# Performance work log

Hardware: AMD Instinct MI355X
Metric: run time of the kernel (lower is better)

Reference implementation:

```python
import jax, jax.numpy as jnp
import numpy as np

WINDOW_SIZE = 11
SIGMA = 1.5
CHANNEL = 3
L = 2.0
C1 = (0.01 * L) ** 2
C2 = (0.03 * L) ** 2
WEIGHTS = jnp.asarray([0.0448, 0.2856, 0.3001, 0.2363, 0.1333], dtype=jnp.float32)


def _create_window(window_size=WINDOW_SIZE, channel=CHANNEL):
    x = jnp.arange(window_size, dtype=jnp.float32)
    g = jnp.exp(-((x - window_size // 2) ** 2) / (2.0 * SIGMA ** 2))
    g = g / g.sum()
    w2d = jnp.outer(g, g)  # (ws, ws)
    # depthwise kernel, OIHW with I=1, O=channel
    return jnp.broadcast_to(w2d[None, None], (channel, 1, window_size, window_size))


def _depthwise_conv(x, w):
    # x: (B,C,H,W), w: (C,1,kh,kw), groups=C, VALID padding
    return jax.lax.conv_general_dilated(
        x, w, window_strides=(1, 1), padding='VALID',
        feature_group_count=x.shape[1],
        dimension_numbers=('NCHW', 'OIHW', 'NCHW'))


def _ssim_level(img1, img2, window):
    mu1 = _depthwise_conv(img1, window)
    mu2 = _depthwise_conv(img2, window)
    mu1_sq = mu1 * mu1
    mu2_sq = mu2 * mu2
    mu1_mu2 = mu1 * mu2
    sigma1_sq = _depthwise_conv(img1 * img1, window) - mu1_sq
    sigma2_sq = _depthwise_conv(img2 * img2, window) - mu2_sq
    sigma12 = _depthwise_conv(img1 * img2, window) - mu1_mu2
    v1 = 2.0 * sigma12 + C2
    v2 = sigma1_sq + sigma2_sq + C2
    cs = jnp.mean(v1 / v2)
    ssim_map = (2.0 * mu1_mu2 + C1) * v1 / ((mu1_sq + mu2_sq + C1) * v2)
    return jnp.mean(ssim_map), cs


def _avg_pool2(x):
    b, c, h, w = x.shape
    return x.reshape(b, c, h // 2, 2, w // 2, 2).mean(axis=(3, 5))


def _msssim(img1, img2):
    window = _create_window()
    mssim, mcs = [], []
    for _ in range(WEIGHTS.shape[0]):
        sim, cs = _ssim_level(img1, img2, window)
        mssim.append(sim)
        mcs.append(cs)
        img1 = _avg_pool2(img1)
        img2 = _avg_pool2(img2)
    mssim = jnp.stack(mssim)
    mcs = jnp.stack(mcs)
    # normalize=True
    mssim = (mssim + 1.0) / 2.0
    mcs = (mcs + 1.0) / 2.0
    pow1 = mcs ** WEIGHTS
    pow2 = mssim ** WEIGHTS
    # faithful to source: prod over broadcast of pow1[:-1] * pow2[-1]
    return jnp.prod(pow1[:-1] * pow2[-1])


def setup_inputs() -> dict:
    key = jax.random.key(0)
    k1, k2 = jax.random.split(key)
    shape = (16, 3, 512, 512)
    output = jax.random.uniform(k1, shape, dtype=jnp.float32)
    gt = jax.random.uniform(k2, shape, dtype=jnp.float32)
    return {"output": output, "gt": gt}


def reference(output, gt):
    return 1.0 - _msssim(output, gt)
```

## Files before the change

### kernel.cpp

```cpp
#include <hip/hip_runtime.h>
#include <math.h>

typedef float vf2 __attribute__((ext_vector_type(2)));

__device__ __forceinline__ vf2 pk_fma(vf2 a, vf2 b, vf2 c) {
    vf2 d;
    asm("v_pk_fma_f32 %0, %1, %2, %3" : "=v"(d) : "v"(a), "v"(b), "v"(c));
    return d;
}
__device__ __forceinline__ vf2 pk_mul(vf2 a, vf2 b) {
    vf2 d;
    asm("v_pk_mul_f32 %0, %1, %2" : "=v"(d) : "v"(a), "v"(b));
    return d;
}
__device__ __forceinline__ vf2 pk_fma_blo(vf2 w, vf2 b, vf2 c) {
    vf2 d;
    asm("v_pk_fma_f32 %0, %1, %2, %3 op_sel_hi:[0,1,1]"
        : "=v"(d) : "v"(w), "v"(b), "v"(c));
    return d;
}
__device__ __forceinline__ vf2 pk_fma_bhi(vf2 w, vf2 b, vf2 c) {
    vf2 d;
    asm("v_pk_fma_f32 %0, %1, %2, %3 op_sel:[1,0,0] op_sel_hi:[1,1,1]"
        : "=v"(d) : "v"(w), "v"(b), "v"(c));
    return d;
}

#define L0_H 512
#define L0_HOUT 502
#define L0_HP 256
#define L0_SEG 64
#define L0_NCHUNK 7
#define ROWW 536
#define NQ 134
#define CARRY_BASE (11 * ROWW)
#define STREAM_WORDS (CARRY_BASE + 2 * ROWW)

__global__ __launch_bounds__(256)
void msssim_stream_l0(const float* __restrict__ img1,
                      const float* __restrict__ img2,
                      double* __restrict__ sums,
                      float* __restrict__ poolP, float* __restrict__ poolQ)
{
    __shared__ __align__(16) float buf[STREAM_WORDS];
    __shared__ float wred[4][2];

    const float gs[11] = {0.00102838f, 0.00759875f, 0.03600077f, 0.10936070f,
                          0.21300554f, 0.26601173f, 0.21300554f, 0.10936070f,
                          0.03600077f, 0.00759875f, 0.00102838f};

    const int tid = threadIdx.x;
    const int c0 = blockIdx.x * 256;
    const int oy0 = blockIdx.y * L0_SEG;
    const long long plane = (long long)blockIdx.z * L0_H * L0_H;
    const long long pplane = (long long)blockIdx.z * L0_HP * L0_HP;
    const bool colok = (c0 + tid) < L0_HOUT;

    const int par = tid & 1;
    vf2 wp[6];
    #pragma unroll
    for (int jq = 0; jq < 6; ++jq) {
        const int i0 = 2 * jq, i1 = 2 * jq + 1;
        const float we0 = (i0 < 11) ? gs[i0] : 0.f;
        const float wo0 = (i0 >= 1) ? gs[i0 - 1] : 0.f;
        const float we1 = (i1 < 11) ? gs[i1] : 0.f;
        const float wo1 = (i1 >= 1) ? gs[i1 - 1] : 0.f;
        wp[jq].x = par ? wo0 : we0;
        wp[jq].y = par ? wo1 : we1;
    }
    vf2 wgv[6];
    #pragma unroll
    for (int k = 0; k < 6; ++k) { wgv[k].x = gs[k]; wgv[k].y = gs[k]; }

    int rowS[6], colS[6], ldsoff[6], rHS[6];
    #pragma unroll
    for (int t = 0; t < 6; ++t) {
        const int s = tid + 256 * t;
        if (s < 11 * NQ) {
            const int r = s / NQ, q = s - NQ * r;
            rowS[t] = r;
            colS[t] = c0 + 2 * q;
            ldsoff[t] = r * ROWW + q * 4;
            rHS[t] = r * L0_H;
        } else { rowS[t] = -1; colS[t] = 0; ldsoff[t] = 0; rHS[t] = 0; }
    }

    float4 pf[6];
    auto prefetch = [&](int ybase) {
        const int yH = ybase * L0_H;
        #pragma unroll
        for (int t = 0; t < 6; ++t) {
            float2 a = make_float2(0.f, 0.f), b = make_float2(0.f, 0.f);
            if (rowS[t] >= 0) {
                const int y = ybase + rowS[t];
                if (y < L0_H && colS[t] < L0_H) {
                    const long long idx = plane + yH + rHS[t] + colS[t];
                    a = *(const float2*)(img1 + idx);
                    b = *(const float2*)(img2 + idx);
                }
            }
            pf[t] = make_float4(a.x + b.x, a.x - b.x, a.y + b.y, a.y - b.y);
        }
    };
    auto stage_write = [&]() {
        #pragma unroll
        for (int t = 0; t < 6; ++t)
            if (rowS[t] >= 0) *(float4*)&buf[ldsoff[t]] = pf[t];
    };

    prefetch(oy0);
    stage_write();
    __syncthreads();

    vf2 pd_pq[11], pd_sq[11];
    #pragma unroll
    for (int s = 0; s < 11; ++s) { pd_pq[s] = (vf2){0.f, 0.f}; pd_sq[s] = (vf2){0.f, 0.f}; }

    const int qb4 = (tid >> 1) * 4;
    const float C1 = 4.0e-4f, C2 = 3.6e-3f;
    float ssim_acc = 0.f, cs_acc = 0.f;

    for (int c = 0; c < L0_NCHUNK; ++c) {
        const int cs = oy0 + 11 * c;
        const bool more = (c + 1 < L0_NCHUNK);

        if (more) prefetch(cs + 11);

        if (tid < 128) {
            const int px = (c0 >> 1) + tid;
            const int t4 = tid * 4;
            for (int jp = (cs & 1); jp + 1 <= 10; jp += 2) {
                const int py = (cs + jp) >> 1;
                if (py < L0_HP) {
                    const float4 v0 = *(const float4*)&buf[jp * ROWW + t4];
                    const float4 v1 = *(const float4*)&buf[(jp + 1) * ROWW + t4];
                    poolP[pplane + py * L0_HP + px] = 0.25f * (v0.x + v0.z + v1.x + v1.z);
                    poolQ[pplane + py * L0_HP + px] = 0.25f * (v0.y + v0.w + v1.y + v1.w);
                }
            }
            if (c > 0 && (cs & 1)) {
                const int py = (cs - 1) >> 1;
                if (py < L0_HP) {
                    const float4 v0 = *(const float4*)&buf[CARRY_BASE + ((c - 1) & 1) * ROWW + t4];
                    const float4 v1 = *(const float4*)&buf[t4];
                    poolP[pplane + py * L0_HP + px] = 0.25f * (v0.x + v0.z + v1.x + v1.z);
                    poolQ[pplane + py * L0_HP + px] = 0.25f * (v0.y + v0.w + v1.y + v1.w);
                }
            }
        }
        if (((cs & 1) == 0) && more && tid < NQ) {
            *(float4*)&buf[CARRY_BASE + (c & 1) * ROWW + tid * 4] =
                *(const float4*)&buf[10 * ROWW + tid * 4];
        }

        #pragma unroll
        for (int j = 0; j < 11; ++j) {
            pd_pq[j] = (vf2){0.f, 0.f};
            pd_sq[j] = (vf2){0.f, 0.f};

            float4 q[6];
            const int rw = j * ROWW + qb4;
            #pragma unroll
            for (int u = 0; u < 6; ++u) q[u] = *(const float4*)&buf[rw + 4 * u];

            vf2 hpq = {0.f, 0.f}, hsq = {0.f, 0.f};
            #pragma unroll
            for (int u = 0; u < 6; ++u) {
                const vf2 elo = {q[u].x, q[u].y};
                const vf2 ehi = {q[u].z, q[u].w};
                const vf2 slo = pk_mul(elo, elo);
                const vf2 shi = pk_mul(ehi, ehi);
                hpq = pk_fma_blo(wp[u], elo, hpq);
                hpq = pk_fma_bhi(wp[u], ehi, hpq);
                hsq = pk_fma_blo(wp[u], slo, hsq);
                hsq = pk_fma_bhi(wp[u], shi, hsq);
            }
            #pragma unroll
            for (int k = 0; k < 11; ++k) {
                const int s = (j - k + 11) % 11;
                const int m = (k <= 5) ? k : 10 - k;
                pd_pq[s] = pk_fma(wgv[m], hpq, pd_pq[s]);
                pd_sq[s] = pk_fma(wgv[m], hsq, pd_sq[s]);
            }
            const int yrel = 11 * c + j;
            if (yrel >= 10) {
                const int s = (j + 1) % 11;
                const int orow = yrel - 10;
                if (orow < L0_SEG && (oy0 + orow) < L0_HOUT && colok) {
                    const vf2 musq = pk_mul(pd_pq[s], pd_pq[s]);
                    const float sP = pd_sq[s].x - musq.x;
                    const float sQ = pd_sq[s].y - musq.y;
                    const float v1 = 0.5f * (sP - sQ) + C2;
                    const float v2 = 0.5f * (sP + sQ) + C2;
                    const float num1 = 0.5f * (musq.x - musq.y) + C1;
                    const float den1 = 0.5f * (musq.x + musq.y) + C1;
                    cs_acc += v1 * __builtin_amdgcn_rcpf(v2);
                    ssim_acc += num1 * v1 * __builtin_amdgcn_rcpf(den1 * v2);
                }
            }
        }

        __syncthreads();
        if (more) stage_write();
        __syncthreads();
    }

    #pragma unroll
    for (int off = 32; off > 0; off >>= 1) {
        ssim_acc += __shfl_down(ssim_acc, off);
        cs_acc   += __shfl_down(cs_acc, off);
    }
    const int wave = tid >> 6;
    if ((tid & 63) == 0) { wred[wave][0] = ssim_acc; wred[wave][1] = cs_acc; }
    __syncthreads();
    if (tid == 0) {
        atomicAdd(&sums[0], (double)(wred[0][0] + wred[1][0] + wred[2][0] + wred[3][0]));
        atomicAdd(&sums[5], (double)(wred[0][1] + wred[1][1] + wred[2][1] + wred[3][1]));
    }
}

#define TILE 32
#define IN_DIM 42
#define SCP 21
#define HALO 10
#define STAGE_WORDS (IN_DIM * SCP * 4)
#define SH 340
#define HB STAGE_WORDS
#define SMEM_WORDS (HB + 16 * SH)

__global__ __launch_bounds__(256)
void msssim_level_kernel(const float* __restrict__ src1,
                         const float* __restrict__ src2,
                         int H, int level, int tiles_per_seg, int pq_input,
                         double* __restrict__ sums,
                         float* __restrict__ pool1, float* __restrict__ pool2)
{
    __shared__ __align__(16) float smem[SMEM_WORDS];
    __shared__ float wred[4][2];

    const float g[11] = {0.00102838f, 0.00759875f, 0.03600077f, 0.10936070f,
                         0.21300554f, 0.26601173f, 0.21300554f, 0.10936070f,
                         0.03600077f, 0.00759875f, 0.00102838f};
    vf2 wg[11];
    #pragma unroll
    for (int k = 0; k < 11; ++k) { wg[k].x = g[k]; wg[k].y = g[k]; }

    const int tid = threadIdx.x;
    const int Hout = H - HALO;
    const int ntiles = (Hout + TILE - 1) / TILE;
    const int tstart = blockIdx.y * tiles_per_seg;
    const int tend = min(ntiles, tstart + tiles_per_seg);
    const int ox0 = blockIdx.x * TILE;
    const int Hp = H >> 1;
    const long long base = (long long)blockIdx.z * H * H;

    int rHS[4], rS[4], xS[4];
    #pragma unroll
    for (int t4 = 0; t4 < 4; ++t4) {
        const int s = tid + 256 * t4;
        if (s < IN_DIM * SCP) {
            const int r = s / SCP, cp = s - r * SCP;
            rS[t4] = r; rHS[t4] = r * H; xS[t4] = ox0 + 2 * cp;
        } else { rS[t4] = -1; rHS[t4] = 0; xS[t4] = 0; }
    }

    auto load_slot = [&](int t4, int ybase) -> float4 {
        float2 a = make_float2(0.f, 0.f), b = make_float2(0.f, 0.f);
        if (rS[t4] >= 0) {
            const int y = ybase + rS[t4], x = xS[t4];
            if (y < H && x < H) {
                const long long idx = base + (long long)ybase * H + rHS[t4] + x;
                a = *(const float2*)(src1 + idx);
                b = *(const float2*)(src2 + idx);
            }
        }
        if (pq_input) return make_float4(a.x, b.x, a.y, b.y);
        return make_float4(a.x + b.x, a.x - b.x, a.y + b.y, a.y - b.y);
    };

    float4 pref[4];
    {
        #pragma unroll
        for (int t4 = 0; t4 < 4; ++t4) pref[t4] = load_slot(t4, tstart * TILE);
        #pragma unroll
        for (int t4 = 0; t4 < 4; ++t4)
            if (rS[t4] >= 0) *(float4*)&smem[(tid + 256 * t4) * 4] = pref[t4];
    }
    __syncthreads();

    float ssim_acc = 0.f, cs_acc = 0.f;

    for (int tt = tstart; tt < tend; ++tt) {
        const int ty0 = tt * TILE;
        const bool more = (tt + 1 < tend);

        if (more) {
            #pragma unroll
            for (int t4 = 0; t4 < 4; ++t4) pref[t4] = load_slot(t4, ty0 + TILE);
        }

        if (pool1 != nullptr) {
            const int pr = tid >> 4, pc = tid & 15;
            const int py = (ty0 >> 1) + pr, px = (ox0 >> 1) + pc;
            if (py < Hp && px < Hp) {
                const float4 v0 = *(const float4*)&smem[(2 * pr * SCP + pc) * 4];
                const float4 v1 = *(const float4*)&smem[((2 * pr + 1) * SCP + pc) * 4];
                const long long ob = (long long)blockIdx.z * Hp * Hp + (long long)py * Hp + px;
                pool1[ob] = 0.25f * (v0.x + v0.z + v1.x + v1.z);
                pool2[ob] = 0.25f * (v0.y + v0.w + v1.y + v1.w);
            }
        }

        float4 hA[3], hBv[3];
        #pragma unroll
        for (int t = 0; t < 3; ++t) {
            const int p = tid + 256 * t;
            if (p < IN_DIM * 16) {
                const int r = p >> 4, m = p & 15;
                vf2 Apq = {0.f, 0.f}, Asq = {0.f, 0.f};
                vf2 Bpq = {0.f, 0.f}, Bsq = {0.f, 0.f};
                #pragma unroll
                for (int jj = 0; jj < 6; ++jj) {
                    const float4 v = *(const float4*)&smem[(r * SCP + m + jj) * 4];
                    const vf2 lo = {v.x, v.y};
                    const vf2 hi = {v.z, v.w};
                    const vf2 losq = pk_mul(lo, lo);
                    const vf2 hisq = pk_mul(hi, hi);
                    Apq = pk_fma(wg[2 * jj], lo, Apq);
                    Asq = pk_fma(wg[2 * jj], losq, Asq);
                    if (jj >= 1) {
                        Bpq = pk_fma(wg[2 * jj - 1], lo, Bpq);
                        Bsq = pk_fma(wg[2 * jj - 1], losq, Bsq);
                    }
                    if (jj <= 4) {
                        Apq = pk_fma(wg[2 * jj + 1], hi, Apq);
                        Asq = pk_fma(wg[2 * jj + 1], hisq, Asq);
                    }
                    Bpq = pk_fma(wg[2 * jj], hi, Bpq);
                    Bsq = pk_fma(wg[2 * jj], hisq, Bsq);
                }
                hA[t]  = make_float4(Apq.x, Apq.y, Asq.x, Asq.y);
                hBv[t] = make_float4(Bpq.x, Bpq.y, Bsq.x, Bsq.y);
            }
        }
        __syncthreads();

        #pragma unroll
        for (int t = 0; t < 3; ++t) {
            const int p = tid + 256 * t;
            if (p < IN_DIM * 16) {
                const int r = p >> 4, m = p & 15;
                const int hb = HB + m * SH + r * 8;
                *(float4*)&smem[hb]     = hA[t];
                *(float4*)&smem[hb + 4] = hBv[t];
            }
        }
        if (more) {
            #pragma unroll
            for (int t4 = 0; t4 < 4; ++t4)
                if (rS[t4] >= 0) *(float4*)&smem[(tid + 256 * t4) * 4] = pref[t4];
        }
        __syncthreads();

        const int tx = tid & 31, rg = tid >> 5;
        const int r0 = rg * 4;
        const int m = tx >> 1, par = tx & 1;
        const int hb = HB + m * SH + par * 4;

        vf2 accPQ[4], accSQ[4];
        #pragma unroll
        for (int o = 0; o < 4; ++o) {
            accPQ[o] = (vf2){0.f, 0.f};
            accSQ[o] = (vf2){0.f, 0.f};
        }
        #pragma unroll
        for (int i = 0; i < 14; ++i) {
            const float4 h4 = *(const float4*)&smem[hb + (r0 + i) * 8];
            const vf2 ppq = {h4.x, h4.y};
            const vf2 psq = {h4.z, h4.w};
            #pragma unroll
            for (int o = 0; o < 4; ++o) {
                const int k = i - o;
                if (k >= 0 && k <= 10) {
                    accPQ[o] = pk_fma(wg[k], ppq, accPQ[o]);
                    accSQ[o] = pk_fma(wg[k], psq, accSQ[o]);
                }
            }
        }

        const float C1 = 4.0e-4f;
        const float C2 = 3.6e-3f;
        const int ox = ox0 + tx;
        #pragma unroll
        for (int o = 0; o < 4; ++o) {
            const int oy = ty0 + r0 + o;
            if (oy < Hout && ox < Hout) {
                const vf2 musq = pk_mul(accPQ[o], accPQ[o]);
                const float sP = accSQ[o].x - musq.x;
                const float sQ = accSQ[o].y - musq.y;
                const float v1 = 0.5f * (sP - sQ) + C2;
                const float v2 = 0.5f * (sP + sQ) + C2;
                const float num1 = 0.5f * (musq.x - musq.y) + C1;
                const float den1 = 0.5f * (musq.x + musq.y) + C1;
                cs_acc += v1 * __builtin_amdgcn_rcpf(v2);
                ssim_acc += num1 * v1 * __builtin_amdgcn_rcpf(den1 * v2);
            }
        }
    }

    #pragma unroll
    for (int off = 32; off > 0; off >>= 1) {
        ssim_acc += __shfl_down(ssim_acc, off);
        cs_acc   += __shfl_down(cs_acc, off);
    }
    const int wave = tid >> 6;
    if ((tid & 63) == 0) { wred[wave][0] = ssim_acc; wred[wave][1] = cs_acc; }
    __syncthreads();
    if (tid == 0) {
        const float s = wred[0][0] + wred[1][0] + wred[2][0] + wred[3][0];
        const float c = wred[0][1] + wred[1][1] + wred[2][1] + wred[3][1];
        atomicAdd(&sums[level],     (double)s);
        atomicAdd(&sums[5 + level], (double)c);
    }
}

__global__ void msssim_final_kernel(const double* __restrict__ sums,
                                    float* __restrict__ out)
{
    if (threadIdx.x == 0 && blockIdx.x == 0) {
        const double W[5] = {0.0448, 0.2856, 0.3001, 0.2363, 0.1333};
        const int Houts[5] = {502, 246, 118, 54, 22};
        double mssim[5], mcs[5];
        for (int l = 0; l < 5; ++l) {
            const double cnt = 48.0 * (double)Houts[l] * (double)Houts[l];
            mssim[l] = (sums[l]     / cnt + 1.0) * 0.5;
            mcs[l]   = (sums[5 + l] / cnt + 1.0) * 0.5;
        }
        const double p2 = pow(mssim[4], W[4]);
        double prod = 1.0;
        for (int l = 0; l < 4; ++l) prod *= pow(mcs[l], W[l]) * p2;
        out[0] = (float)(1.0 - prod);
    }
}

extern "C" void kernel_launch(void* const* d_in, const int* in_sizes, int n_in,
                              void* d_out, int out_size, void* d_ws, size_t ws_size,
                              hipStream_t stream)
{
    const float* img1 = (const float*)d_in[0];
    const float* img2 = (const float*)d_in[1];
    float* out = (float*)d_out;
    (void)in_sizes; (void)n_in; (void)out_size; (void)ws_size;

    char* ws = (char*)d_ws;
    double* sums = (double*)ws;
    float* X1 = (float*)(ws + 256);
    float* X2 = X1 + 3145728;
    float* Y1 = X2 + 3145728;
    float* Y2 = Y1 + 786432;

    hipMemsetAsync(sums, 0, 10 * sizeof(double), stream);

    hipLaunchKernelGGL(msssim_stream_l0, dim3(2, 8, 48), dim3(256), 0, stream,
                       img1, img2, sums, X1, X2);

    auto launch_level = [&](const float* a, const float* b, int H, int level,
                            int segs, float* pa, float* pb) {
        const int Hout = H - HALO;
        const int strips = (Hout + TILE - 1) / TILE;
        const int ntiles = (Hout + TILE - 1) / TILE;
        const int tps = (ntiles + segs - 1) / segs;
        dim3 grid(strips, segs, 48);
        hipLaunchKernelGGL(msssim_level_kernel, grid, dim3(256), 0, stream,
                           a, b, H, level, tps, 1, sums, pa, pb);
    };

    launch_level(X1, X2, 256, 1, 2, Y1, Y2);
    launch_level(Y1, Y2, 128, 2, 4, X1, X2);
    launch_level(X1, X2, 64, 3, 2, Y1, Y2);
    launch_level(Y1, Y2, 32, 4, 1, nullptr, nullptr);

    hipLaunchKernelGGL(msssim_final_kernel, dim3(1), dim3(64), 0, stream, sums, out);
}
```

Before: 142.7 us.

## Precompute pyramid in one cascade kernel and run all SSIM levels in one launch

Replaces the chain of per-level launches with two kernels. The first computes every pooled pyramid level from the inputs in one pass, using shared memory for the intermediate levels. The second is a single launch whose blocks are split across all five SSIM levels, with level 1 pooling directly from the full-resolution inputs. This removes serial launch dependencies and the small, low-occupancy launches for the coarse levels. In exchange the inputs are read again by the cascade kernel and by level 1, and the grid mixes blocks with very different amounts of work.

Measured after the change: 129.8 us. -9.1%, faster.

```diff
diff --git a/kernel.cpp b/kernel.cpp
--- a/kernel.cpp
+++ b/kernel.cpp
@@ -28,168 +28,381 @@
 
 #define L0_H 512
 #define L0_HOUT 502
-#define L0_HP 256
 #define L0_SEG 64
 #define L0_NCHUNK 7
 #define ROWW 536
 #define NQ 134
-#define CARRY_BASE (11 * ROWW)
-#define STREAM_WORDS (CARRY_BASE + 2 * ROWW)
+#define L0_BUF (11 * ROWW)
+
+#define TILE 32
+#define IN_DIM 42
+#define SCP 21
+#define HALO 10
+#define LV_STAGE (IN_DIM * SCP * 4)
+#define SH 340
+#define HB LV_STAGE
+#define MEGA_WORDS (HB + 16 * SH)
 
 __global__ __launch_bounds__(256)
-void msssim_stream_l0(const float* __restrict__ img1,
-                      const float* __restrict__ img2,
-                      double* __restrict__ sums,
-                      float* __restrict__ poolP, float* __restrict__ poolQ)
+void msssim_cascade(const float* __restrict__ img1, const float* __restrict__ img2,
+                    float* __restrict__ Y1, float* __restrict__ Y2,
+                    float* __restrict__ Z1, float* __restrict__ Z2,
+                    float* __restrict__ W1, float* __restrict__ W2)
 {
-    __shared__ __align__(16) float buf[STREAM_WORDS];
+    __shared__ float xs[16 * 256 * 2];
+    __shared__ float ysh[8 * 128 * 2];
+    __shared__ float zsh[4 * 64 * 2];
+    const int tid = threadIdx.x;
+    const int reg = blockIdx.x & 15, plane = blockIdx.x >> 4;
+    const long long obase = (long long)plane * 262144;
+
+    for (int i = tid; i < 16 * 256; i += 256) {
+        const int r = i >> 8, c = i & 255;
+        const long long o = obase + (long long)(2 * (16 * reg + r)) * 512 + 2 * c;
+        const float2 a0 = *(const float2*)&img1[o];
+        const float2 a1 = *(const float2*)&img1[o + 512];
+        const float2 b0 = *(const float2*)&img2[o];
+        const float2 b1 = *(const float2*)&img2[o + 512];
+        xs[2 * i]     = 0.25f * ((a0.x + b0.x) + (a0.y + b0.y) + (a1.x + b1.x) + (a1.y + b1.y));
+        xs[2 * i + 1] = 0.25f * ((a0.x - b0.x) + (a0.y - b0.y) + (a1.x - b1.x) + (a1.y - b1.y));
+    }
+    __syncthreads();
+    for (int i = tid; i < 8 * 128; i += 256) {
+        const int r = i >> 7, c = i & 127;
+        const int i00 = ((2 * r) * 256 + 2 * c) * 2;
+        const float yP = 0.25f * (xs[i00] + xs[i00 + 2] + xs[i00 + 512] + xs[i00 + 514]);
+        const float yQ = 0.25f * (xs[i00 + 1] + xs[i00 + 3] + xs[i00 + 513] + xs[i00 + 515]);
+        ysh[2 * i] = yP; ysh[2 * i + 1] = yQ;
+        const long long yo = (long long)plane * 16384 + (long long)(8 * reg + r) * 128 + c;
+        Y1[yo] = yP; Y2[yo] = yQ;
+    }
+    __syncthreads();
+    for (int i = tid; i < 4 * 64; i += 256) {
+        const int r = i >> 6, c = i & 63;
+        const int i00 = ((2 * r) * 128 + 2 * c) * 2;
+        const float zP = 0.25f * (ysh[i00] + ysh[i00 + 2] + ysh[i00 + 256] + ysh[i00 + 258]);
+        const float zQ = 0.25f * (ysh[i00 + 1] + ysh[i00 + 3] + ysh[i00 + 257] + ysh[i00 + 259]);
+        zsh[2 * i] = zP; zsh[2 * i + 1] = zQ;
+        const long long zo = (long long)plane * 4096 + (long long)(4 * reg + r) * 64 + c;
+        Z1[zo] = zP; Z2[zo] = zQ;
+    }
+    __syncthreads();
+    for (int i = tid; i < 2 * 32; i += 256) {
+        const int r = i >> 5, c = i & 31;
+        const int i00 = ((2 * r) * 64 + 2 * c) * 2;
+        const long long wo = (long long)plane * 1024 + (long long)(2 * reg + r) * 32 + c;
+        W1[wo] = 0.25f * (zsh[i00] + zsh[i00 + 2] + zsh[i00 + 128] + zsh[i00 + 130]);
+        W2[wo] = 0.25f * (zsh[i00 + 1] + zsh[i00 + 3] + zsh[i00 + 129] + zsh[i00 + 131]);
+    }
+}
+
+__global__ __launch_bounds__(256)
+void msssim_mega(const float* __restrict__ img1, const float* __restrict__ img2,
+                 const float* __restrict__ Y1, const float* __restrict__ Y2,
+                 const float* __restrict__ Z1, const float* __restrict__ Z2,
+                 const float* __restrict__ W1, const float* __restrict__ W2,
+                 double* __restrict__ sums)
+{
+    __shared__ __align__(16) float smem[MEGA_WORDS];
     __shared__ float wred[4][2];
 
     const float gs[11] = {0.00102838f, 0.00759875f, 0.03600077f, 0.10936070f,
                           0.21300554f, 0.26601173f, 0.21300554f, 0.10936070f,
                           0.03600077f, 0.00759875f, 0.00102838f};
-
     const int tid = threadIdx.x;
-    const int c0 = blockIdx.x * 256;
-    const int oy0 = blockIdx.y * L0_SEG;
-    const long long plane = (long long)blockIdx.z * L0_H * L0_H;
-    const long long pplane = (long long)blockIdx.z * L0_HP * L0_HP;
-    const bool colok = (c0 + tid) < L0_HOUT;
-
-    const int par = tid & 1;
-    vf2 wp[6];
-    #pragma unroll
-    for (int jq = 0; jq < 6; ++jq) {
-        const int i0 = 2 * jq, i1 = 2 * jq + 1;
-        const float we0 = (i0 < 11) ? gs[i0] : 0.f;
-        const float wo0 = (i0 >= 1) ? gs[i0 - 1] : 0.f;
-        const float we1 = (i1 < 11) ? gs[i1] : 0.f;
-        const float wo1 = (i1 >= 1) ? gs[i1 - 1] : 0.f;
-        wp[jq].x = par ? wo0 : we0;
-        wp[jq].y = par ? wo1 : we1;
-    }
-    vf2 wgv[6];
-    #pragma unroll
-    for (int k = 0; k < 6; ++k) { wgv[k].x = gs[k]; wgv[k].y = gs[k]; }
-
-    int rowS[6], colS[6], ldsoff[6], rHS[6];
-    #pragma unroll
-    for (int t = 0; t < 6; ++t) {
-        const int s = tid + 256 * t;
-        if (s < 11 * NQ) {
-            const int r = s / NQ, q = s - NQ * r;
-            rowS[t] = r;
-            colS[t] = c0 + 2 * q;
-            ldsoff[t] = r * ROWW + q * 4;
-            rHS[t] = r * L0_H;
-        } else { rowS[t] = -1; colS[t] = 0; ldsoff[t] = 0; rHS[t] = 0; }
-    }
-
-    float4 pf[6];
-    auto prefetch = [&](int ybase) {
-        const int yH = ybase * L0_H;
-        #pragma unroll
-        for (int t = 0; t < 6; ++t) {
-            float2 a = make_float2(0.f, 0.f), b = make_float2(0.f, 0.f);
-            if (rowS[t] >= 0) {
-                const int y = ybase + rowS[t];
-                if (y < L0_H && colS[t] < L0_H) {
-                    const long long idx = plane + yH + rHS[t] + colS[t];
-                    a = *(const float2*)(img1 + idx);
-                    b = *(const float2*)(img2 + idx);
-                }
-            }
-            pf[t] = make_float4(a.x + b.x, a.x - b.x, a.y + b.y, a.y - b.y);
-        }
-    };
-    auto stage_write = [&]() {
-        #pragma unroll
-        for (int t = 0; t < 6; ++t)
-            if (rowS[t] >= 0) *(float4*)&buf[ldsoff[t]] = pf[t];
-    };
-
-    prefetch(oy0);
-    stage_write();
-    __syncthreads();
-
-    vf2 pd_pq[11], pd_sq[11];
-    #pragma unroll
-    for (int s = 0; s < 11; ++s) { pd_pq[s] = (vf2){0.f, 0.f}; pd_sq[s] = (vf2){0.f, 0.f}; }
-
-    const int qb4 = (tid >> 1) * 4;
+    const int bid = blockIdx.x;
     const float C1 = 4.0e-4f, C2 = 3.6e-3f;
     float ssim_acc = 0.f, cs_acc = 0.f;
-
-    for (int c = 0; c < L0_NCHUNK; ++c) {
-        const int cs = oy0 + 11 * c;
-        const bool more = (c + 1 < L0_NCHUNK);
-
-        if (more) prefetch(cs + 11);
-
-        if (tid < 128) {
-            const int px = (c0 >> 1) + tid;
-            const int t4 = tid * 4;
-            for (int jp = (cs & 1); jp + 1 <= 10; jp += 2) {
-                const int py = (cs + jp) >> 1;
-                if (py < L0_HP) {
-                    const float4 v0 = *(const float4*)&buf[jp * ROWW + t4];
-                    const float4 v1 = *(const float4*)&buf[(jp + 1) * ROWW + t4];
-                    poolP[pplane + py * L0_HP + px] = 0.25f * (v0.x + v0.z + v1.x + v1.z);
-                    poolQ[pplane + py * L0_HP + px] = 0.25f * (v0.y + v0.w + v1.y + v1.w);
-                }
-            }
-            if (c > 0 && (cs & 1)) {
-                const int py = (cs - 1) >> 1;
-                if (py < L0_HP) {
-                    const float4 v0 = *(const float4*)&buf[CARRY_BASE + ((c - 1) & 1) * ROWW + t4];
-                    const float4 v1 = *(const float4*)&buf[t4];
-                    poolP[pplane + py * L0_HP + px] = 0.25f * (v0.x + v0.z + v1.x + v1.z);
-                    poolQ[pplane + py * L0_HP + px] = 0.25f * (v0.y + v0.w + v1.y + v1.w);
-                }
-            }
-        }
-        if (((cs & 1) == 0) && more && tid < NQ) {
-            *(float4*)&buf[CARRY_BASE + (c & 1) * ROWW + tid * 4] =
-                *(const float4*)&buf[10 * ROWW + tid * 4];
-        }
-
-        #pragma unroll
-        for (int j = 0; j < 11; ++j) {
-            pd_pq[j] = (vf2){0.f, 0.f};
-            pd_sq[j] = (vf2){0.f, 0.f};
-
-            float4 q[6];
-            const int rw = j * ROWW + qb4;
-            #pragma unroll
-            for (int u = 0; u < 6; ++u) q[u] = *(const float4*)&buf[rw + 4 * u];
-
-            vf2 hpq = {0.f, 0.f}, hsq = {0.f, 0.f};
-            #pragma unroll
-            for (int u = 0; u < 6; ++u) {
-                const vf2 elo = {q[u].x, q[u].y};
-                const vf2 ehi = {q[u].z, q[u].w};
-                const vf2 slo = pk_mul(elo, elo);
-                const vf2 shi = pk_mul(ehi, ehi);
-                hpq = pk_fma_blo(wp[u], elo, hpq);
-                hpq = pk_fma_bhi(wp[u], ehi, hpq);
-                hsq = pk_fma_blo(wp[u], slo, hsq);
-                hsq = pk_fma_bhi(wp[u], shi, hsq);
-            }
-            #pragma unroll
-            for (int k = 0; k < 11; ++k) {
-                const int s = (j - k + 11) % 11;
-                const int m = (k <= 5) ? k : 10 - k;
-                pd_pq[s] = pk_fma(wgv[m], hpq, pd_pq[s]);
-                pd_sq[s] = pk_fma(wgv[m], hsq, pd_sq[s]);
-            }
-            const int yrel = 11 * c + j;
-            if (yrel >= 10) {
-                const int s = (j + 1) % 11;
-                const int orow = yrel - 10;
-                if (orow < L0_SEG && (oy0 + orow) < L0_HOUT && colok) {
-                    const vf2 musq = pk_mul(pd_pq[s], pd_pq[s]);
-                    const float sP = pd_sq[s].x - musq.x;
-                    const float sQ = pd_sq[s].y - musq.y;
+    int level;
+
+    if (bid < 768) {
+        level = 0;
+        const int c0 = (bid & 1) * 256;
+        const int oy0 = ((bid >> 1) & 7) * L0_SEG;
+        const long long plane = (long long)(bid >> 4) * 262144;
+        const bool colok = (c0 + tid) < L0_HOUT;
+
+        const int par = tid & 1;
+        vf2 wp[6];
+        #pragma unroll
+        for (int jq = 0; jq < 6; ++jq) {
+            const int i0 = 2 * jq, i1 = 2 * jq + 1;
+            const float we0 = (i0 < 11) ? gs[i0] : 0.f;
+            const float wo0 = (i0 >= 1) ? gs[i0 - 1] : 0.f;
+            const float we1 = (i1 < 11) ? gs[i1] : 0.f;
+            const float wo1 = (i1 >= 1) ? gs[i1 - 1] : 0.f;
+            wp[jq].x = par ? wo0 : we0;
+            wp[jq].y = par ? wo1 : we1;
+        }
+        vf2 wgv[6];
+        #pragma unroll
+        for (int k = 0; k < 6; ++k) { wgv[k].x = gs[k]; wgv[k].y = gs[k]; }
+
+        int rowS[6], colS[6], ldsoff[6], rHS[6];
+        #pragma unroll
+        for (int t = 0; t < 6; ++t) {
+            const int s = tid + 256 * t;
+            if (s < 11 * NQ) {
+                const int r = s / NQ, q = s - NQ * r;
+                rowS[t] = r; colS[t] = c0 + 2 * q;
+                ldsoff[t] = r * ROWW + q * 4; rHS[t] = r * L0_H;
+            } else { rowS[t] = -1; colS[t] = 0; ldsoff[t] = 0; rHS[t] = 0; }
+        }
+
+        float4 pf[6];
+        auto prefetch = [&](int ybase) {
+            const int yH = ybase * L0_H;
+            #pragma unroll
+            for (int t = 0; t < 6; ++t) {
+                float2 a = make_float2(0.f, 0.f), b = make_float2(0.f, 0.f);
+                if (rowS[t] >= 0) {
+                    const int y = ybase + rowS[t];
+                    if (y < L0_H && colS[t] < L0_H) {
+                        const long long idx = plane + yH + rHS[t] + colS[t];
+                        a = *(const float2*)(img1 + idx);
+                        b = *(const float2*)(img2 + idx);
+                    }
+                }
+                pf[t] = make_float4(a.x + b.x, a.x - b.x, a.y + b.y, a.y - b.y);
+            }
+        };
+        auto stage_write = [&]() {
+            #pragma unroll
+            for (int t = 0; t < 6; ++t)
+                if (rowS[t] >= 0) *(float4*)&smem[ldsoff[t]] = pf[t];
+        };
+
+        prefetch(oy0);
+        stage_write();
+        __syncthreads();
+
+        vf2 pd_pq[11], pd_sq[11];
+        #pragma unroll
+        for (int s = 0; s < 11; ++s) { pd_pq[s] = (vf2){0.f, 0.f}; pd_sq[s] = (vf2){0.f, 0.f}; }
+
+        const int qb4 = (tid >> 1) * 4;
+
+        for (int c = 0; c < L0_NCHUNK; ++c) {
+            const bool more = (c + 1 < L0_NCHUNK);
+            if (more) prefetch(oy0 + 11 * (c + 1));
+
+            #pragma unroll
+            for (int j = 0; j < 11; ++j) {
+                pd_pq[j] = (vf2){0.f, 0.f};
+                pd_sq[j] = (vf2){0.f, 0.f};
+
+                float4 q[6];
+                const int rw = j * ROWW + qb4;
+                #pragma unroll
+                for (int u = 0; u < 6; ++u) q[u] = *(const float4*)&smem[rw + 4 * u];
+
+                vf2 hpq = {0.f, 0.f}, hsq = {0.f, 0.f};
+                #pragma unroll
+                for (int u = 0; u < 6; ++u) {
+                    const vf2 elo = {q[u].x, q[u].y};
+                    const vf2 ehi = {q[u].z, q[u].w};
+                    const vf2 slo = pk_mul(elo, elo);
+                    const vf2 shi = pk_mul(ehi, ehi);
+                    hpq = pk_fma_blo(wp[u], elo, hpq);
+                    hpq = pk_fma_bhi(wp[u], ehi, hpq);
+                    hsq = pk_fma_blo(wp[u], slo, hsq);
+                    hsq = pk_fma_bhi(wp[u], shi, hsq);
+                }
+                #pragma unroll
+                for (int k = 0; k < 11; ++k) {
+                    const int s = (j - k + 11) % 11;
+                    const int m = (k <= 5) ? k : 10 - k;
+                    pd_pq[s] = pk_fma(wgv[m], hpq, pd_pq[s]);
+                    pd_sq[s] = pk_fma(wgv[m], hsq, pd_sq[s]);
+                }
+                const int yrel = 11 * c + j;
+                if (yrel >= 10) {
+                    const int s = (j + 1) % 11;
+                    const int orow = yrel - 10;
+                    if (orow < L0_SEG && (oy0 + orow) < L0_HOUT && colok) {
+                        const vf2 musq = pk_mul(pd_pq[s], pd_pq[s]);
+                        const float sP = pd_sq[s].x - musq.x;
+                        const float sQ = pd_sq[s].y - musq.y;
+                        const float v1 = 0.5f * (sP - sQ) + C2;
+                        const float v2 = 0.5f * (sP + sQ) + C2;
+                        const float num1 = 0.5f * (musq.x - musq.y) + C1;
+                        const float den1 = 0.5f * (musq.x + musq.y) + C1;
+                        cs_acc += v1 * __builtin_amdgcn_rcpf(v2);
+                        ssim_acc += num1 * v1 * __builtin_amdgcn_rcpf(den1 * v2);
+                    }
+                }
+            }
+
+            __syncthreads();
+            if (more) stage_write();
+            __syncthreads();
+        }
+    } else {
+        const int id = bid - 768;
+        const float *src1 = nullptr, *src2 = nullptr;
+        int H, strip, seg, plane, tps;
+        if (id < 768) {
+            level = 1; H = 256; tps = 4;
+            plane = id >> 4; const int t = id & 15; strip = t & 7; seg = t >> 3;
+        } else if (id < 1536) {
+            level = 2; H = 128; tps = 1; src1 = Y1; src2 = Y2;
+            const int r = id - 768; plane = r >> 4; const int t = r & 15; strip = t & 3; seg = t >> 2;
+        } else if (id < 1728) {
+            level = 3; H = 64; tps = 1; src1 = Z1; src2 = Z2;
+            const int r = id - 1536; plane = r >> 2; const int t = r & 3; strip = t & 1; seg = t >> 1;
+        } else {
+            level = 4; H = 32; tps = 1; src1 = W1; src2 = W2;
+            plane = id - 1728; strip = 0; seg = 0;
+        }
+
+        vf2 wg[11];
+        #pragma unroll
+        for (int k = 0; k < 11; ++k) { wg[k].x = gs[k]; wg[k].y = gs[k]; }
+
+        const int Hout = H - HALO;
+        const int ntiles = (Hout + TILE - 1) / TILE;
+        const int tstart = seg * tps;
+        const int tend = min(ntiles, tstart + tps);
+        const int ox0 = strip * TILE;
+        const long long base = (long long)plane * H * H;
+        const long long obase = (long long)plane * 262144;
+
+        int rHS[4], rS[4], xS[4];
+        #pragma unroll
+        for (int t4 = 0; t4 < 4; ++t4) {
+            const int s = tid + 256 * t4;
+            if (s < IN_DIM * SCP) {
+                const int r = s / SCP, cp = s - r * SCP;
+                rS[t4] = r; rHS[t4] = r * H; xS[t4] = ox0 + 2 * cp;
+            } else { rS[t4] = -1; rHS[t4] = 0; xS[t4] = 0; }
+        }
+
+        auto load_slot = [&](int t4, int ybase) -> float4 {
+            if (rS[t4] < 0) return make_float4(0.f, 0.f, 0.f, 0.f);
+            const int y = ybase + rS[t4], x = xS[t4];
+            if (y >= H || x >= H) return make_float4(0.f, 0.f, 0.f, 0.f);
+            if (level == 1) {
+                const long long o = obase + (long long)(2 * y) * 512 + 2 * x;
+                const float4 A0 = *(const float4*)(img1 + o);
+                const float4 A1 = *(const float4*)(img1 + o + 512);
+                const float4 B0 = *(const float4*)(img2 + o);
+                const float4 B1 = *(const float4*)(img2 + o + 512);
+                const float P0 = 0.25f * ((A0.x + B0.x) + (A0.y + B0.y) + (A1.x + B1.x) + (A1.y + B1.y));
+                const float Q0 = 0.25f * ((A0.x - B0.x) + (A0.y - B0.y) + (A1.x - B1.x) + (A1.y - B1.y));
+                const float P1 = 0.25f * ((A0.z + B0.z) + (A0.w + B0.w) + (A1.z + B1.z) + (A1.w + B1.w));
+                const float Q1 = 0.25f * ((A0.z - B0.z) + (A0.w - B0.w) + (A1.z - B1.z) + (A1.w - B1.w));
+                return make_float4(P0, Q0, P1, Q1);
+            }
+            const long long idx = base + (long long)ybase * H + rHS[t4] + x;
+            const float2 a = *(const float2*)(src1 + idx);
+            const float2 b = *(const float2*)(src2 + idx);
+            return make_float4(a.x, b.x, a.y, b.y);
+        };
+
+        float4 pref[4];
+        {
+            #pragma unroll
+            for (int t4 = 0; t4 < 4; ++t4) pref[t4] = load_slot(t4, tstart * TILE);
+            #pragma unroll
+            for (int t4 = 0; t4 < 4; ++t4)
+                if (rS[t4] >= 0) *(float4*)&smem[(tid + 256 * t4) * 4] = pref[t4];
+        }
+        __syncthreads();
+
+        for (int tt = tstart; tt < tend; ++tt) {
+            const int ty0 = tt * TILE;
+            const bool more = (tt + 1 < tend);
+
+            if (more) {
+                #pragma unroll
+                for (int t4 = 0; t4 < 4; ++t4) pref[t4] = load_slot(t4, ty0 + TILE);
+            }
+
+            float4 hA[3], hBv[3];
+            #pragma unroll
+            for (int t = 0; t < 3; ++t) {
+                const int p = tid + 256 * t;
+                if (p < IN_DIM * 16) {
+                    const int r = p >> 4, m = p & 15;
+                    vf2 Apq = {0.f, 0.f}, Asq = {0.f, 0.f};
+                    vf2 Bpq = {0.f, 0.f}, Bsq = {0.f, 0.f};
+                    #pragma unroll
+                    for (int jj = 0; jj < 6; ++jj) {
+                        const float4 v = *(const float4*)&smem[(r * SCP + m + jj) * 4];
+                        const vf2 lo = {v.x, v.y};
+                        const vf2 hi = {v.z, v.w};
+                        const vf2 losq = pk_mul(lo, lo);
+                        const vf2 hisq = pk_mul(hi, hi);
+                        Apq = pk_fma(wg[2 * jj], lo, Apq);
+                        Asq = pk_fma(wg[2 * jj], losq, Asq);
+                        if (jj >= 1) {
+                            Bpq = pk_fma(wg[2 * jj - 1], lo, Bpq);
+                            Bsq = pk_fma(wg[2 * jj - 1], losq, Bsq);
+                        }
+                        if (jj <= 4) {
+                            Apq = pk_fma(wg[2 * jj + 1], hi, Apq);
+                            Asq = pk_fma(wg[2 * jj + 1], hisq, Asq);
+                        }
+                        Bpq = pk_fma(wg[2 * jj], hi, Bpq);
+                        Bsq = pk_fma(wg[2 * jj], hisq, Bsq);
+                    }
+                    hA[t]  = make_float4(Apq.x, Apq.y, Asq.x, Asq.y);
+                    hBv[t] = make_float4(Bpq.x, Bpq.y, Bsq.x, Bsq.y);
+                }
+            }
+            __syncthreads();
+
+            #pragma unroll
+            for (int t = 0; t < 3; ++t) {
+                const int p = tid + 256 * t;
+                if (p < IN_DIM * 16) {
+                    const int r = p >> 4, m = p & 15;
+                    const int hb = HB + m * SH + r * 8;
+                    *(float4*)&smem[hb]     = hA[t];
+                    *(float4*)&smem[hb + 4] = hBv[t];
+                }
+            }
+            if (more) {
+                #pragma unroll
+                for (int t4 = 0; t4 < 4; ++t4)
+                    if (rS[t4] >= 0) *(float4*)&smem[(tid + 256 * t4) * 4] = pref[t4];
+            }
+            __syncthreads();
+
+            const int tx = tid & 31, rg = tid >> 5;
+            const int r0 = rg * 4;
+            const int m = tx >> 1, par = tx & 1;
+            const int hb = HB + m * SH + par * 4;
+
+            vf2 accPQ[4], accSQ[4];
+            #pragma unroll
+            for (int o = 0; o < 4; ++o) {
+                accPQ[o] = (vf2){0.f, 0.f};
+                accSQ[o] = (vf2){0.f, 0.f};
+            }
+            #pragma unroll
+            for (int i = 0; i < 14; ++i) {
+                const float4 h4 = *(const float4*)&smem[hb + (r0 + i) * 8];
+                const vf2 ppq = {h4.x, h4.y};
+                const vf2 psq = {h4.z, h4.w};
+                #pragma unroll
+                for (int o = 0; o < 4; ++o) {
+                    const int k = i - o;
+                    if (k >= 0 && k <= 10) {
+                        accPQ[o] = pk_fma(wg[k], ppq, accPQ[o]);
+                        accSQ[o] = pk_fma(wg[k], psq, accSQ[o]);
+                    }
+                }
+            }
+
+            const int ox = ox0 + tx;
+            #pragma unroll
+            for (int o = 0; o < 4; ++o) {
+                const int oy = ty0 + r0 + o;
+                if (oy < Hout && ox < Hout) {
+                    const vf2 musq = pk_mul(accPQ[o], accPQ[o]);
+                    const float sP = accSQ[o].x - musq.x;
+                    const float sQ = accSQ[o].y - musq.y;
                     const float v1 = 0.5f * (sP - sQ) + C2;
                     const float v2 = 0.5f * (sP + sQ) + C2;
                     const float num1 = 0.5f * (musq.x - musq.y) + C1;
@@ -197,213 +410,6 @@
                     cs_acc += v1 * __builtin_amdgcn_rcpf(v2);
                     ssim_acc += num1 * v1 * __builtin_amdgcn_rcpf(den1 * v2);
                 }
-            }
-        }
-
-        __syncthreads();
-        if (more) stage_write();
-        __syncthreads();
-    }
-
-    #pragma unroll
-    for (int off = 32; off > 0; off >>= 1) {
-        ssim_acc += __shfl_down(ssim_acc, off);
-        cs_acc   += __shfl_down(cs_acc, off);
-    }
-    const int wave = tid >> 6;
-    if ((tid & 63) == 0) { wred[wave][0] = ssim_acc; wred[wave][1] = cs_acc; }
-    __syncthreads();
-    if (tid == 0) {
-        atomicAdd(&sums[0], (double)(wred[0][0] + wred[1][0] + wred[2][0] + wred[3][0]));
-        atomicAdd(&sums[5], (double)(wred[0][1] + wred[1][1] + wred[2][1] + wred[3][1]));
-    }
-}
-
-#define TILE 32
-#define IN_DIM 42
-#define SCP 21
-#define HALO 10
-#define STAGE_WORDS (IN_DIM * SCP * 4)
-#define SH 340
-#define HB STAGE_WORDS
-#define SMEM_WORDS (HB + 16 * SH)
-
-__global__ __launch_bounds__(256)
-void msssim_level_kernel(const float* __restrict__ src1,
-                         const float* __restrict__ src2,
-                         int H, int level, int tiles_per_seg, int pq_input,
-                         double* __restrict__ sums,
-                         float* __restrict__ pool1, float* __restrict__ pool2)
-{
-    __shared__ __align__(16) float smem[SMEM_WORDS];
-    __shared__ float wred[4][2];
-
-    const float g[11] = {0.00102838f, 0.00759875f, 0.03600077f, 0.10936070f,
-                         0.21300554f, 0.26601173f, 0.21300554f, 0.10936070f,
-                         0.03600077f, 0.00759875f, 0.00102838f};
-    vf2 wg[11];
-    #pragma unroll
-    for (int k = 0; k < 11; ++k) { wg[k].x = g[k]; wg[k].y = g[k]; }
-
-    const int tid = threadIdx.x;
-    const int Hout = H - HALO;
-    const int ntiles = (Hout + TILE - 1) / TILE;
-    const int tstart = blockIdx.y * tiles_per_seg;
-    const int tend = min(ntiles, tstart + tiles_per_seg);
-    const int ox0 = blockIdx.x * TILE;
-    const int Hp = H >> 1;
-    const long long base = (long long)blockIdx.z * H * H;
-
-    int rHS[4], rS[4], xS[4];
-    #pragma unroll
-    for (int t4 = 0; t4 < 4; ++t4) {
-        const int s = tid + 256 * t4;
-        if (s < IN_DIM * SCP) {
-            const int r = s / SCP, cp = s - r * SCP;
-            rS[t4] = r; rHS[t4] = r * H; xS[t4] = ox0 + 2 * cp;
-        } else { rS[t4] = -1; rHS[t4] = 0; xS[t4] = 0; }
-    }
-
-    auto load_slot = [&](int t4, int ybase) -> float4 {
-        float2 a = make_float2(0.f, 0.f), b = make_float2(0.f, 0.f);
-        if (rS[t4] >= 0) {
-            const int y = ybase + rS[t4], x = xS[t4];
-            if (y < H && x < H) {
-                const long long idx = base + (long long)ybase * H + rHS[t4] + x;
-                a = *(const float2*)(src1 + idx);
-                b = *(const float2*)(src2 + idx);
-            }
-        }
-        if (pq_input) return make_float4(a.x, b.x, a.y, b.y);
-        return make_float4(a.x + b.x, a.x - b.x, a.y + b.y, a.y - b.y);
-    };
-
-    float4 pref[4];
-    {
-        #pragma unroll
-        for (int t4 = 0; t4 < 4; ++t4) pref[t4] = load_slot(t4, tstart * TILE);
-        #pragma unroll
-        for (int t4 = 0; t4 < 4; ++t4)
-            if (rS[t4] >= 0) *(float4*)&smem[(tid + 256 * t4) * 4] = pref[t4];
-    }
-    __syncthreads();
-
-    float ssim_acc = 0.f, cs_acc = 0.f;
-
-    for (int tt = tstart; tt < tend; ++tt) {
-        const int ty0 = tt * TILE;
-        const bool more = (tt + 1 < tend);
-
-        if (more) {
-            #pragma unroll
-            for (int t4 = 0; t4 < 4; ++t4) pref[t4] = load_slot(t4, ty0 + TILE);
-        }
-
-        if (pool1 != nullptr) {
-            const int pr = tid >> 4, pc = tid & 15;
-            const int py = (ty0 >> 1) + pr, px = (ox0 >> 1) + pc;
-            if (py < Hp && px < Hp) {
-                const float4 v0 = *(const float4*)&smem[(2 * pr * SCP + pc) * 4];
-                const float4 v1 = *(const float4*)&smem[((2 * pr + 1) * SCP + pc) * 4];
-                const long long ob = (long long)blockIdx.z * Hp * Hp + (long long)py * Hp + px;
-                pool1[ob] = 0.25f * (v0.x + v0.z + v1.x + v1.z);
-                pool2[ob] = 0.25f * (v0.y + v0.w + v1.y + v1.w);
-            }
-        }
-
-        float4 hA[3], hBv[3];
-        #pragma unroll
-        for (int t = 0; t < 3; ++t) {
-            const int p = tid + 256 * t;
-            if (p < IN_DIM * 16) {
-                const int r = p >> 4, m = p & 15;
-                vf2 Apq = {0.f, 0.f}, Asq = {0.f, 0.f};
-                vf2 Bpq = {0.f, 0.f}, Bsq = {0.f, 0.f};
-                #pragma unroll
-                for (int jj = 0; jj < 6; ++jj) {
-                    const float4 v = *(const float4*)&smem[(r * SCP + m + jj) * 4];
-                    const vf2 lo = {v.x, v.y};
-                    const vf2 hi = {v.z, v.w};
-                    const vf2 losq = pk_mul(lo, lo);
-                    const vf2 hisq = pk_mul(hi, hi);
-                    Apq = pk_fma(wg[2 * jj], lo, Apq);
-                    Asq = pk_fma(wg[2 * jj], losq, Asq);
-                    if (jj >= 1) {
-                        Bpq = pk_fma(wg[2 * jj - 1], lo, Bpq);
-                        Bsq = pk_fma(wg[2 * jj - 1], losq, Bsq);
-                    }
-                    if (jj <= 4) {
-                        Apq = pk_fma(wg[2 * jj + 1], hi, Apq);
-                        Asq = pk_fma(wg[2 * jj + 1], hisq, Asq);
-                    }
-                    Bpq = pk_fma(wg[2 * jj], hi, Bpq);
-                    Bsq = pk_fma(wg[2 * jj], hisq, Bsq);
-                }
-                hA[t]  = make_float4(Apq.x, Apq.y, Asq.x, Asq.y);
-                hBv[t] = make_float4(Bpq.x, Bpq.y, Bsq.x, Bsq.y);
-            }
-        }
-        __syncthreads();
-
-        #pragma unroll
-        for (int t = 0; t < 3; ++t) {
-            const int p = tid + 256 * t;
-            if (p < IN_DIM * 16) {
-                const int r = p >> 4, m = p & 15;
-                const int hb = HB + m * SH + r * 8;
-                *(float4*)&smem[hb]     = hA[t];
-                *(float4*)&smem[hb + 4] = hBv[t];
-            }
-        }
-        if (more) {
-            #pragma unroll
-            for (int t4 = 0; t4 < 4; ++t4)
-                if (rS[t4] >= 0) *(float4*)&smem[(tid + 256 * t4) * 4] = pref[t4];
-        }
-        __syncthreads();
-
-        const int tx = tid & 31, rg = tid >> 5;
-        const int r0 = rg * 4;
-        const int m = tx >> 1, par = tx & 1;
-        const int hb = HB + m * SH + par * 4;
-
-        vf2 accPQ[4], accSQ[4];
-        #pragma unroll
-        for (int o = 0; o < 4; ++o) {
-            accPQ[o] = (vf2){0.f, 0.f};
-            accSQ[o] = (vf2){0.f, 0.f};
-        }
-        #pragma unroll
-        for (int i = 0; i < 14; ++i) {
-            const float4 h4 = *(const float4*)&smem[hb + (r0 + i) * 8];
-            const vf2 ppq = {h4.x, h4.y};
-            const vf2 psq = {h4.z, h4.w};
-            #pragma unroll
-            for (int o = 0; o < 4; ++o) {
-                const int k = i - o;
-                if (k >= 0 && k <= 10) {
-                    accPQ[o] = pk_fma(wg[k], ppq, accPQ[o]);
-                    accSQ[o] = pk_fma(wg[k], psq, accSQ[o]);
-                }
-            }
-        }
-
-        const float C1 = 4.0e-4f;
-        const float C2 = 3.6e-3f;
-        const int ox = ox0 + tx;
-        #pragma unroll
-        for (int o = 0; o < 4; ++o) {
-            const int oy = ty0 + r0 + o;
-            if (oy < Hout && ox < Hout) {
-                const vf2 musq = pk_mul(accPQ[o], accPQ[o]);
-                const float sP = accSQ[o].x - musq.x;
-                const float sQ = accSQ[o].y - musq.y;
-                const float v1 = 0.5f * (sP - sQ) + C2;
-                const float v2 = 0.5f * (sP + sQ) + C2;
-                const float num1 = 0.5f * (musq.x - musq.y) + C1;
-                const float den1 = 0.5f * (musq.x + musq.y) + C1;
-                cs_acc += v1 * __builtin_amdgcn_rcpf(v2);
-                ssim_acc += num1 * v1 * __builtin_amdgcn_rcpf(den1 * v2);
             }
         }
     }
@@ -454,31 +460,20 @@
 
     char* ws = (char*)d_ws;
     double* sums = (double*)ws;
-    float* X1 = (float*)(ws + 256);
-    float* X2 = X1 + 3145728;
-    float* Y1 = X2 + 3145728;
+    float* Y1 = (float*)(ws + 256);
     float* Y2 = Y1 + 786432;
+    float* Z1 = Y2 + 786432;
+    float* Z2 = Z1 + 196608;
+    float* W1 = Z2 + 196608;
+    float* W2 = W1 + 49152;
 
     hipMemsetAsync(sums, 0, 10 * sizeof(double), stream);
 
-    hipLaunchKernelGGL(msssim_stream_l0, dim3(2, 8, 48), dim3(256), 0, stream,
-                       img1, img2, sums, X1, X2);
-
-    auto launch_level = [&](const float* a, const float* b, int H, int level,
-                            int segs, float* pa, float* pb) {
-        const int Hout = H - HALO;
-        const int strips = (Hout + TILE - 1) / TILE;
-        const int ntiles = (Hout + TILE - 1) / TILE;
-        const int tps = (ntiles + segs - 1) / segs;
-        dim3 grid(strips, segs, 48);
-        hipLaunchKernelGGL(msssim_level_kernel, grid, dim3(256), 0, stream,
-                           a, b, H, level, tps, 1, sums, pa, pb);
-    };
-
-    launch_level(X1, X2, 256, 1, 2, Y1, Y2);
-    launch_level(Y1, Y2, 128, 2, 4, X1, X2);
-    launch_level(X1, X2, 64, 3, 2, Y1, Y2);
-    launch_level(Y1, Y2, 32, 4, 1, nullptr, nullptr);
+    hipLaunchKernelGGL(msssim_cascade, dim3(768), dim3(256), 0, stream,
+                       img1, img2, Y1, Y2, Z1, Z2, W1, W2);
+
+    hipLaunchKernelGGL(msssim_mega, dim3(2544), dim3(256), 0, stream,
+                       img1, img2, Y1, Y2, Z1, Z2, W1, W2, sums);
 
     hipLaunchKernelGGL(msssim_final_kernel, dim3(1), dim3(64), 0, stream, sums, out);
 }
```
